# Optimization experiments

Hardware: AMD Instinct MI355X
Metric: run time of the kernel (lower is better)

The kernel has to match this reference:

```python
import jax, jax.numpy as jnp
import numpy as np

N = 100_000      # nodes
E = 1_600_000    # edges (avg degree 16)
IN = 128         # in_features
F = 64           # out_features
H = 1            # num_heads (module's broadcasting only valid for H==1)
S = 1            # num_samples
SLOPE = 0.2      # leaky relu negative slope


def setup_inputs() -> dict:
    key = jax.random.key(0)
    ks = jax.random.split(key, 6)
    feat = jax.random.normal(ks[0], (N, IN), jnp.float32)
    src = jax.random.randint(ks[1], (E,), 0, N)
    dst = jax.random.randint(ks[2], (E,), 0, N)
    noise = jax.random.normal(ks[3], (E, S, H, 1), jnp.float32)  # rsample noise
    W_fc = jax.random.normal(ks[4], (IN, H * F), jnp.float32) / np.sqrt(IN)
    W_post = jax.random.normal(ks[5], (F, 4), jnp.float32) / np.sqrt(F)
    b_post = jnp.zeros((4,), jnp.float32)
    bias = jnp.zeros((H, F), jnp.float32)
    return dict(feat=feat, W_fc=W_fc, W_post=W_post, b_post=b_post,
                bias=bias, noise=noise, src=src, dst=dst)


def reference(feat, W_fc, W_post, b_post, bias, noise, src, dst):
    # node projection: [N, IN] -> [N, H, F]
    h = (feat @ W_fc).reshape(N, H, F)
    # posterior params: [N, H, 4] -> four [N, H, 1]
    pp = h @ W_post + b_post
    loc_l, loc_r, lsl, lsr = jnp.split(pp, 4, axis=-1)
    # per-edge u_add_v gathers
    loc_e = loc_l[src] + loc_r[dst]                       # [E, H, 1]
    loc_e = jnp.where(loc_e >= 0, loc_e, SLOPE * loc_e)   # leaky relu
    scale_e = jnp.exp(lsl[src] + lsr[dst])                # [E, H, 1]
    # reparameterized sample: [E, S, H, 1]
    e = loc_e[:, None] + scale_e[:, None] * noise
    # edge softmax over incoming edges of each dst node
    emax = jax.ops.segment_max(e, dst, num_segments=N)
    e_exp = jnp.exp(e - emax[dst])
    esum = jax.ops.segment_sum(e_exp, dst, num_segments=N)
    a = e_exp / esum[dst]                                 # [E, S, H, 1]
    a = jnp.swapaxes(a, 1, -1)                            # [E, 1, H, S]
    # u_mul_e then scatter-sum to dst: [E, H, F, 1] * [E, 1, H, S]
    m = h[src][..., None] * a                             # [E, H, F, S] (H==1)
    rst = jax.ops.segment_sum(m, dst, num_segments=N)     # [N, H, F, S]
    return rst + bias[..., None]
```

## Files before the change

### kernel.cpp

```cpp
#include <hip/hip_runtime.h>
#include <math.h>

#define NSLOPE 0.2f
#define ASTRIDE 136
#define CSH 10
#define NCB 128
#define EPB 2048
#define K4T 512
#define EPT 4
#define FSPLIT 16
#define SCH 1152

typedef __attribute__((ext_vector_type(8))) short bf16x8;
typedef __attribute__((ext_vector_type(4))) short bf16x4;
typedef __attribute__((ext_vector_type(4))) float f32x4;

__device__ __forceinline__ unsigned short f2bf(float x) {
    unsigned u = __float_as_uint(x);
    u += 0x7fffu + ((u >> 16) & 1u);
    return (unsigned short)(u >> 16);
}

__global__ __launch_bounds__(128) void kW(const float* __restrict__ wfc,
                                          const float* __restrict__ wpost,
                                          float4* __restrict__ wc) {
    __shared__ float wp_s[256];
    int t = threadIdx.x;
    wp_s[t] = wpost[t];
    wp_s[128 + t] = wpost[128 + t];
    __syncthreads();
    float a0 = 0.f, a1 = 0.f, a2 = 0.f, a3 = 0.f;
    for (int n = 0; n < 64; n++) {
        float w = wfc[t * 64 + n];
        a0 += w * wp_s[n * 4 + 0]; a1 += w * wp_s[n * 4 + 1];
        a2 += w * wp_s[n * 4 + 2]; a3 += w * wp_s[n * 4 + 3];
    }
    float4 o; o.x = a0; o.y = a1; o.z = a2; o.w = a3;
    wc[t] = o;
}

__global__ __launch_bounds__(256) void k1_mfma(
    const float* __restrict__ feat, const float* __restrict__ wfc,
    float4* __restrict__ h_g, int n)
{
    __shared__ unsigned short a_s[64 * ASTRIDE];
    __shared__ unsigned short b_s[64 * ASTRIDE];
    int t = threadIdx.x;
    int row0 = blockIdx.x * 64;
    for (int i = t; i < 2048; i += 256) {
        int row = i >> 5, c4 = (i & 31) * 4;
        float4 f = {0.f, 0.f, 0.f, 0.f};
        if (row0 + row < n) f = ((const float4*)(feat + (long)(row0 + row) * 128))[i & 31];
        bf16x4 b4;
        b4.x = (short)f2bf(f.x); b4.y = (short)f2bf(f.y);
        b4.z = (short)f2bf(f.z); b4.w = (short)f2bf(f.w);
        *(bf16x4*)(a_s + row * ASTRIDE + c4) = b4;
    }
    for (int i = t; i < 2048; i += 256) {
        int k = i >> 4, n0 = (i & 15) * 4;
        float4 f = ((const float4*)wfc)[i];
        b_s[(n0 + 0) * ASTRIDE + k] = f2bf(f.x);
        b_s[(n0 + 1) * ASTRIDE + k] = f2bf(f.y);
        b_s[(n0 + 2) * ASTRIDE + k] = f2bf(f.z);
        b_s[(n0 + 3) * ASTRIDE + k] = f2bf(f.w);
    }
    __syncthreads();
    int lane = t & 63, wv = t >> 6;
    int c = lane & 15, quad = lane >> 4;
    f32x4 acc[4] = {{0.f,0.f,0.f,0.f},{0.f,0.f,0.f,0.f},{0.f,0.f,0.f,0.f},{0.f,0.f,0.f,0.f}};
    int arow = wv * 16 + c;
    #pragma unroll
    for (int kb = 0; kb < 4; kb++) {
        int ko = kb * 32 + quad * 8;
        bf16x8 af = *(const bf16x8*)(a_s + arow * ASTRIDE + ko);
        #pragma unroll
        for (int tt = 0; tt < 4; tt++) {
            bf16x8 bf = *(const bf16x8*)(b_s + (tt * 16 + c) * ASTRIDE + ko);
            acc[tt] = __builtin_amdgcn_mfma_f32_16x16x32_bf16(af, bf, acc[tt], 0, 0, 0);
        }
    }
    __syncthreads();
    unsigned short* h_s = a_s;
    #pragma unroll
    for (int tt = 0; tt < 4; tt++)
        #pragma unroll
        for (int r = 0; r < 4; r++)
            h_s[(wv * 16 + quad * 4 + r) * 64 + tt * 16 + c] = f2bf(acc[tt][r]);
    __syncthreads();
    for (int i = t; i < 512; i += 256) {
        int row = i >> 3;
        if (row0 + row < n)
            h_g[(long)(row0 + row) * 8 + (i & 7)] = *(const float4*)(h_s + row * 64 + (i & 7) * 8);
    }
}

__global__ __launch_bounds__(256) void k1b_pp(
    const float* __restrict__ feat, const float4* __restrict__ wc,
    const float* __restrict__ bpost, float4* __restrict__ pp,
    int* __restrict__ gcnt, int* __restrict__ fcnt, int NC, int N)
{
    int gid = blockIdx.x * 256 + threadIdx.x;
    if (gid < NC) gcnt[gid] = 0;
    if (gid < NC * 16) fcnt[gid] = 0;
    int wid = gid >> 6;
    int lane = threadIdx.x & 63;
    if (wid >= N) return;
    const float* fr = feat + (long)wid * 128;
    float f0 = fr[lane], f1 = fr[64 + lane];
    float4 w0 = wc[lane], w1 = wc[64 + lane];
    float p0 = f0 * w0.x + f1 * w1.x;
    float p1 = f0 * w0.y + f1 * w1.y;
    float p2 = f0 * w0.z + f1 * w1.z;
    float p3 = f0 * w0.w + f1 * w1.w;
    #pragma unroll
    for (int off = 1; off < 64; off <<= 1) {
        p0 += __shfl_xor(p0, off);
        p1 += __shfl_xor(p1, off);
        p2 += __shfl_xor(p2, off);
        p3 += __shfl_xor(p3, off);
    }
    if (lane == 0) {
        float4 bp = *((const float4*)bpost);
        float4 o;
        o.x = p0 + bp.x; o.y = p1 + bp.y; o.z = p2 + bp.z; o.w = p3 + bp.w;
        pp[wid] = o;
    }
}

__global__ __launch_bounds__(K4T) void k4a(
    const int* __restrict__ src, const int* __restrict__ dst,
    const float* __restrict__ noise, const float4* __restrict__ pp,
    int* __restrict__ gcnt, float2* __restrict__ cbuf, int E, int NC, int CCAP)
{
    __shared__ float    s_ev[EPB];
    __shared__ unsigned s_key[EPB];
    __shared__ unsigned char s_bin[EPB];
    __shared__ int hist[NCB], lbase[NCB], lcur[NCB], gdelta[NCB];
    __shared__ int wtot;
    int t = threadIdx.x;
    long e0 = (long)blockIdx.x * EPB;
    int d[EPT]; bool ok[EPT];
    for (int i = t; i < NCB; i += K4T) hist[i] = 0;
    __syncthreads();
    #pragma unroll
    for (int u = 0; u < EPT; u++) {
        long e = e0 + t + u * K4T;
        ok[u] = e < E;
        d[u] = ok[u] ? __builtin_nontemporal_load(dst + e) : 0;
        if (ok[u]) atomicAdd(&hist[d[u] >> CSH], 1);
    }
    __syncthreads();
    int v = (t < NCB) ? hist[t] : 0;
    int inc = v;
    #pragma unroll
    for (int off = 1; off < 64; off <<= 1) {
        int u2 = __shfl_up(inc, off);
        if ((t & 63) >= off) inc += u2;
    }
    if (t == 63) wtot = inc;
    __syncthreads();
    if (t < NCB) {
        int base = (t >= 64) ? wtot : 0;
        int lb = inc - v + base;
        lbase[t] = lb; lcur[t] = lb;
        if (t < NC && v > 0) {
            int gb = atomicAdd(&gcnt[t], v);
            gdelta[t] = gb - lb;
        }
    }
    __syncthreads();
    #pragma unroll
    for (int u = 0; u < EPT; u++) {
        if (!ok[u]) continue;
        long e = e0 + t + u * K4T;
        int s = __builtin_nontemporal_load(src + e);
        float nz = __builtin_nontemporal_load(noise + e);
        float4 ps = pp[s], pd = pp[d[u]];
        float loc = ps.x + pd.y;
        loc = loc >= 0.f ? loc : NSLOPE * loc;
        float ev = loc + __expf(ps.z + pd.w) * nz;
        int bin = d[u] >> CSH;
        int pos = atomicAdd(&lcur[bin], 1);
        s_ev[pos] = ev;
        s_key[pos] = (unsigned)s | ((unsigned)(d[u] & 1023) << 17);
        s_bin[pos] = (unsigned char)bin;
    }
    __syncthreads();
    long rem = (long)E - e0;
    int btot = rem < EPB ? (int)rem : EPB;
    for (int i = t; i < btot; i += K4T) {
        int bin = s_bin[i];
        int gpos = gdelta[bin] + i;
        if (gpos < CCAP) {
            float2 r; r.x = s_ev[i]; r.y = __uint_as_float(s_key[i]);
            cbuf[(long)bin * CCAP + gpos] = r;
        }
    }
}

__global__ __launch_bounds__(256) void k4b(
    const int* __restrict__ gcnt, const float2* __restrict__ cbuf,
    int* __restrict__ fcnt, float2* __restrict__ fbuf, int CCAP, int FCAP)
{
    __shared__ float    s_ev[SCH], s_ev2[SCH];
    __shared__ unsigned s_key[SCH], s_sr2[SCH];
    __shared__ unsigned char s_sub[SCH], s_sub2[SCH];
    __shared__ int h16[16], b16[16], cur16[16], gd16[16];
    int t = threadIdx.x;
    int c = blockIdx.x >> 4, j = blockIdx.x & 15;
    int cnt = gcnt[c]; if (cnt > CCAP) cnt = CCAP;
    int chunk = (cnt + FSPLIT - 1) / FSPLIT;
    int i0 = j * chunk;
    int i1 = i0 + chunk; if (i1 > cnt) i1 = cnt;
    int n = i1 - i0; if (n < 0) n = 0;
    if (t < 16) { h16[t] = 0; cur16[t] = 0; }
    __syncthreads();
    for (int i = t; i < n; i += 256) {
        float2 r = cbuf[(long)c * CCAP + i0 + i];
        unsigned key = __float_as_uint(r.y);
        int sub = (key >> 23) & 15;
        s_ev[i] = r.x; s_key[i] = key; s_sub[i] = (unsigned char)sub;
        atomicAdd(&h16[sub], 1);
    }
    __syncthreads();
    if (t == 0) {
        int run = 0;
        #pragma unroll
        for (int p = 0; p < 16; p++) { b16[p] = run; run += h16[p]; }
    }
    __syncthreads();
    if (t < 16 && h16[t] > 0)
        gd16[t] = atomicAdd(&fcnt[c * 16 + t], h16[t]) - b16[t];
    __syncthreads();
    for (int i = t; i < n; i += 256) {
        int sub = s_sub[i];
        int pos = b16[sub] + atomicAdd(&cur16[sub], 1);
        unsigned key = s_key[i];
        unsigned s  = key & 0x1FFFFu;
        unsigned dl = (key >> 17) & 63u;
        s_ev2[pos] = s_ev[i];
        s_sr2[pos] = s | (dl << 26);
        s_sub2[pos] = (unsigned char)sub;
    }
    __syncthreads();
    for (int i = t; i < n; i += 256) {
        int sub = s_sub2[i];
        int gpos = gd16[sub] + i;
        if (gpos < FCAP) {
            float2 r; r.x = s_ev2[i]; r.y = __uint_as_float(s_sr2[i]);
            fbuf[(long)(c * 16 + sub) * FCAP + gpos] = r;
        }
    }
}

__global__ __launch_bounds__(256) void k56_node(
    const int* __restrict__ fcnt, const float2* __restrict__ fbuf,
    const uint4* __restrict__ h8, const float* __restrict__ bias,
    float4* __restrict__ out4, int FCAP, int N)
{
    __shared__ float    o_ev[1344 + 8];
    __shared__ unsigned o_sr[1344 + 8];
    __shared__ int c[64], ox[64], c2[64];
    int t = threadIdx.x;
    int b = blockIdx.x;
    int n0 = b << 6;
    int cnt = fcnt[b]; if (cnt > FCAP) cnt = FCAP;
    const float2* rp = fbuf + (long)b * FCAP;
    if (t < 64) { c[t] = 0; c2[t] = 0; }
    __syncthreads();
    for (int i = t; i < cnt; i += 256)
        atomicAdd(&c[__float_as_uint(rp[i].y) >> 26], 1);
    __syncthreads();
    if (t < 64) {
        int val = c[t], inc = val;
        #pragma unroll
        for (int off = 1; off < 64; off <<= 1) {
            int u = __shfl_up(inc, off);
            if (t >= off) inc += u;
        }
        ox[t] = inc - val;
    }
    __syncthreads();
    for (int i = t; i < cnt; i += 256) {
        float2 v = rp[i];
        unsigned pk = __float_as_uint(v.y);
        int dl = pk >> 26;
        int pos = ox[dl] + atomicAdd(&c2[dl], 1);
        o_ev[pos] = v.x;
        o_sr[pos] = pk & 0x03FFFFFFu;
    }
    __syncthreads();
    {
        int nn4 = t >> 2, q = t & 3;
        int cn = c[nn4];
        int i0 = ox[nn4];
        float m = -INFINITY;
        for (int i = q; i < cn; i += 4) m = fmaxf(m, o_ev[i0 + i]);
        m = fmaxf(m, __shfl_xor(m, 1));
        m = fmaxf(m, __shfl_xor(m, 2));
        float ss = 0.f;
        for (int i = q; i < cn; i += 4) {
            float w = __expf(o_ev[i0 + i] - m);
            o_ev[i0 + i] = w;
            ss += w;
        }
        ss += __shfl_xor(ss, 1);
        ss += __shfl_xor(ss, 2);
        float inv = 1.f / ss;
        for (int i = q; i < cn; i += 4) o_ev[i0 + i] *= inv;
    }
    __syncthreads();
    int lane = t & 63, wv = t >> 6;
    int ch = lane & 7, sub = lane >> 3;
    for (int r = 0; r < 16; r += 2) {
        int nnA = wv * 16 + r, nnB = nnA + 1;
        int nodeA = n0 + nnA, nodeB = n0 + nnB;
        int cA = (nodeA < N) ? c[nnA] : 0;
        int cB = (nodeB < N) ? c[nnB] : 0;
        int iA = ox[nnA], iB = ox[nnB];
        float a0[8] = {0.f,0.f,0.f,0.f,0.f,0.f,0.f,0.f};
        float a1[8] = {0.f,0.f,0.f,0.f,0.f,0.f,0.f,0.f};
        int mx = cA > cB ? cA : cB;
        for (int jb = 0; jb < mx; jb += 16) {
            bool vA0 = (jb + sub) < cA, vA1 = (jb + 8 + sub) < cA;
            bool vB0 = (jb + sub) < cB, vB1 = (jb + 8 + sub) < cB;
            int jA0 = vA0 ? iA + jb + sub     : 0;
            int jA1 = vA1 ? iA + jb + 8 + sub : 0;
            int jB0 = vB0 ? iB + jb + sub     : 0;
            int jB1 = vB1 ? iB + jb + 8 + sub : 0;
            float wA0 = vA0 ? o_ev[jA0] : 0.f; int sA0 = vA0 ? (int)o_sr[jA0] : 0;
            float wA1 = vA1 ? o_ev[jA1] : 0.f; int sA1 = vA1 ? (int)o_sr[jA1] : 0;
            float wB0 = vB0 ? o_ev[jB0] : 0.f; int sB0 = vB0 ? (int)o_sr[jB0] : 0;
            float wB1 = vB1 ? o_ev[jB1] : 0.f; int sB1 = vB1 ? (int)o_sr[jB1] : 0;
            uint4 pA0 = h8[(long)sA0 * 8 + ch];
            uint4 pA1 = h8[(long)sA1 * 8 + ch];
            uint4 pB0 = h8[(long)sB0 * 8 + ch];
            uint4 pB1 = h8[(long)sB1 * 8 + ch];
            a0[0] += wA0 * __uint_as_float(pA0.x << 16);
            a0[1] += wA0 * __uint_as_float(pA0.x & 0xffff0000u);
            a0[2] += wA0 * __uint_as_float(pA0.y << 16);
            a0[3] += wA0 * __uint_as_float(pA0.y & 0xffff0000u);
            a0[4] += wA0 * __uint_as_float(pA0.z << 16);
            a0[5] += wA0 * __uint_as_float(pA0.z & 0xffff0000u);
            a0[6] += wA0 * __uint_as_float(pA0.w << 16);
            a0[7] += wA0 * __uint_as_float(pA0.w & 0xffff0000u);
            a0[0] += wA1 * __uint_as_float(pA1.x << 16);
            a0[1] += wA1 * __uint_as_float(pA1.x & 0xffff0000u);
            a0[2] += wA1 * __uint_as_float(pA1.y << 16);
            a0[3] += wA1 * __uint_as_float(pA1.y & 0xffff0000u);
            a0[4] += wA1 * __uint_as_float(pA1.z << 16);
            a0[5] += wA1 * __uint_as_float(pA1.z & 0xffff0000u);
            a0[6] += wA1 * __uint_as_float(pA1.w << 16);
            a0[7] += wA1 * __uint_as_float(pA1.w & 0xffff0000u);
            a1[0] += wB0 * __uint_as_float(pB0.x << 16);
            a1[1] += wB0 * __uint_as_float(pB0.x & 0xffff0000u);
            a1[2] += wB0 * __uint_as_float(pB0.y << 16);
            a1[3] += wB0 * __uint_as_float(pB0.y & 0xffff0000u);
            a1[4] += wB0 * __uint_as_float(pB0.z << 16);
            a1[5] += wB0 * __uint_as_float(pB0.z & 0xffff0000u);
            a1[6] += wB0 * __uint_as_float(pB0.w << 16);
            a1[7] += wB0 * __uint_as_float(pB0.w & 0xffff0000u);
            a1[0] += wB1 * __uint_as_float(pB1.x << 16);
            a1[1] += wB1 * __uint_as_float(pB1.x & 0xffff0000u);
            a1[2] += wB1 * __uint_as_float(pB1.y << 16);
            a1[3] += wB1 * __uint_as_float(pB1.y & 0xffff0000u);
            a1[4] += wB1 * __uint_as_float(pB1.z << 16);
            a1[5] += wB1 * __uint_as_float(pB1.z & 0xffff0000u);
            a1[6] += wB1 * __uint_as_float(pB1.w << 16);
            a1[7] += wB1 * __uint_as_float(pB1.w & 0xffff0000u);
        }
        #pragma unroll
        for (int off = 8; off < 64; off <<= 1)
            #pragma unroll
            for (int i = 0; i < 8; i++) {
                a0[i] += __shfl_xor(a0[i], off);
                a1[i] += __shfl_xor(a1[i], off);
            }
        if (sub == 0) {
            const float* bl = bias + ch * 8;
            if (nodeA < N) {
                f32x4 o0, o1;
                o0[0] = a0[0] + bl[0]; o0[1] = a0[1] + bl[1]; o0[2] = a0[2] + bl[2]; o0[3] = a0[3] + bl[3];
                o1[0] = a0[4] + bl[4]; o1[1] = a0[5] + bl[5]; o1[2] = a0[6] + bl[6]; o1[3] = a0[7] + bl[7];
                __builtin_nontemporal_store(o0, (f32x4*)(out4 + (long)nodeA * 16 + ch * 2));
                __builtin_nontemporal_store(o1, (f32x4*)(out4 + (long)nodeA * 16 + ch * 2 + 1));
            }
            if (nodeB < N) {
                f32x4 o0, o1;
                o0[0] = a1[0] + bl[0]; o0[1] = a1[1] + bl[1]; o0[2] = a1[2] + bl[2]; o0[3] = a1[3] + bl[3];
                o1[0] = a1[4] + bl[4]; o1[1] = a1[5] + bl[5]; o1[2] = a1[6] + bl[6]; o1[3] = a1[7] + bl[7];
                __builtin_nontemporal_store(o0, (f32x4*)(out4 + (long)nodeB * 16 + ch * 2));
                __builtin_nontemporal_store(o1, (f32x4*)(out4 + (long)nodeB * 16 + ch * 2 + 1));
            }
        }
    }
}

extern "C" void kernel_launch(void* const* d_in, const int* in_sizes, int n_in,
                              void* d_out, int out_size, void* d_ws, size_t ws_size,
                              hipStream_t stream) {
    const float* feat  = (const float*)d_in[0];
    const float* wfc   = (const float*)d_in[1];
    const float* wpost = (const float*)d_in[2];
    const float* bpost = (const float*)d_in[3];
    const float* bias  = (const float*)d_in[4];
    const float* noise = (const float*)d_in[5];
    const int*   src   = (const int*)d_in[6];
    const int*   dst   = (const int*)d_in[7];
    int N = in_sizes[0] / 128;
    int E = in_sizes[6];
    int NC = (N + 1023) >> 10;
    int NB = (N + 63) >> 6;
    int ECB = (E + NC - 1) / NC;
    int CCAP = (ECB + 8 * (int)sqrtf((float)ECB) + 71) & ~7;
    int EB  = (int)((long)E * 64 / N);
    int FCAP = (EB + 8 * (int)sqrtf((float)EB) + 39) & ~7;
    if (FCAP > 1344) FCAP = 1344;

    float*  ws   = (float*)d_ws;
    float2* cbuf = (float2*)ws;
    float2* fbuf = (float2*)(ws + (size_t)2 * NC * CCAP);
    float*  h    = ws + (size_t)2 * NC * CCAP + (size_t)2 * NB * FCAP;
    float4* pp   = (float4*)(h + (size_t)32 * N);
    int*    gcnt = (int*)(h + (size_t)32 * N + (size_t)4 * N);
    int*    fcnt = gcnt + 256;
    float4* wc   = (float4*)(fcnt + 2048);

    hipLaunchKernelGGL(kW, dim3(1), dim3(128), 0, stream, wfc, wpost, wc);
    hipLaunchKernelGGL(k1_mfma, dim3((N + 63) / 64), dim3(256), 0, stream,
                       feat, wfc, (float4*)h, N);
    hipLaunchKernelGGL(k1b_pp, dim3((N + 3) / 4), dim3(256), 0, stream,
                       feat, wc, bpost, pp, gcnt, fcnt, NC, N);
    hipLaunchKernelGGL(k4a, dim3((E + EPB - 1) / EPB), dim3(K4T), 0, stream,
                       src, dst, noise, pp, gcnt, cbuf, E, NC, CCAP);
    hipLaunchKernelGGL(k4b, dim3(NC * FSPLIT), dim3(256), 0, stream,
                       gcnt, cbuf, fcnt, fbuf, CCAP, FCAP);
    hipLaunchKernelGGL(k56_node, dim3(NB), dim3(256), 0, stream,
                       fcnt, fbuf, (const uint4*)h, bias, (float4*)d_out, FCAP, N);
}
```

Before: 256.1 us.

## Overlap bucket atomics, cache records in registers, process four nodes per gather pass

Halves the edge-bucketing block size, so blocks are smaller and more numerous. It also defers the global gcnt atomic so its latency overlaps the per-edge compute before the next barrier. In the node kernel, fbuf records are loaded once into registers and reused for both the histogram and scatter passes instead of being read twice from global memory. The aggregation loop now handles four destination nodes per iteration, giving eight independent h8 gathers in flight, which raises register pressure. The register cache assumes at most 1536 records per bucket (6 per thread).

```diff
diff --git a/kernel.cpp b/kernel.cpp
--- a/kernel.cpp
+++ b/kernel.cpp
@@ -5,8 +5,8 @@
 #define ASTRIDE 136
 #define CSH 10
 #define NCB 128
-#define EPB 2048
-#define K4T 512
+#define EPB 1024
+#define K4T 256
 #define EPT 4
 #define FSPLIT 16
 #define SCH 1152
@@ -135,7 +135,7 @@
     __shared__ float    s_ev[EPB];
     __shared__ unsigned s_key[EPB];
     __shared__ unsigned char s_bin[EPB];
-    __shared__ int hist[NCB], lbase[NCB], lcur[NCB], gdelta[NCB];
+    __shared__ int hist[NCB], lcur[NCB], gdelta[NCB];
     __shared__ int wtot;
     int t = threadIdx.x;
     long e0 = (long)blockIdx.x * EPB;
@@ -159,16 +159,15 @@
     }
     if (t == 63) wtot = inc;
     __syncthreads();
+    int lb = 0;
     if (t < NCB) {
         int base = (t >= 64) ? wtot : 0;
-        int lb = inc - v + base;
-        lbase[t] = lb; lcur[t] = lb;
-        if (t < NC && v > 0) {
-            int gb = atomicAdd(&gcnt[t], v);
-            gdelta[t] = gb - lb;
-        }
-    }
-    __syncthreads();
+        lb = inc - v + base;
+        lcur[t] = lb;
+    }
+    __syncthreads();
+    int gb = 0;
+    if (t < NC && v > 0) gb = atomicAdd(&gcnt[t], v);
     #pragma unroll
     for (int u = 0; u < EPT; u++) {
         if (!ok[u]) continue;
@@ -185,6 +184,7 @@
         s_key[pos] = (unsigned)s | ((unsigned)(d[u] & 1023) << 17);
         s_bin[pos] = (unsigned char)bin;
     }
+    if (t < NC && v > 0) gdelta[t] = gb - lb;
     __syncthreads();
     long rem = (long)E - e0;
     int btot = rem < EPB ? (int)rem : EPB;
@@ -268,8 +268,15 @@
     const float2* rp = fbuf + (long)b * FCAP;
     if (t < 64) { c[t] = 0; c2[t] = 0; }
     __syncthreads();
-    for (int i = t; i < cnt; i += 256)
-        atomicAdd(&c[__float_as_uint(rp[i].y) >> 26], 1);
+    float2 rec[6];
+    #pragma unroll
+    for (int j = 0; j < 6; j++) {
+        int i = t + j * 256;
+        if (i < cnt) {
+            rec[j] = rp[i];
+            atomicAdd(&c[__float_as_uint(rec[j].y) >> 26], 1);
+        }
+    }
     __syncthreads();
     if (t < 64) {
         int val = c[t], inc = val;
@@ -281,13 +288,16 @@
         ox[t] = inc - val;
     }
     __syncthreads();
-    for (int i = t; i < cnt; i += 256) {
-        float2 v = rp[i];
-        unsigned pk = __float_as_uint(v.y);
-        int dl = pk >> 26;
-        int pos = ox[dl] + atomicAdd(&c2[dl], 1);
-        o_ev[pos] = v.x;
-        o_sr[pos] = pk & 0x03FFFFFFu;
+    #pragma unroll
+    for (int j = 0; j < 6; j++) {
+        int i = t + j * 256;
+        if (i < cnt) {
+            unsigned pk = __float_as_uint(rec[j].y);
+            int dl = pk >> 26;
+            int pos = ox[dl] + atomicAdd(&c2[dl], 1);
+            o_ev[pos] = rec[j].x;
+            o_sr[pos] = pk & 0x03FFFFFFu;
+        }
     }
     __syncthreads();
     {
@@ -312,85 +322,70 @@
     __syncthreads();
     int lane = t & 63, wv = t >> 6;
     int ch = lane & 7, sub = lane >> 3;
-    for (int r = 0; r < 16; r += 2) {
-        int nnA = wv * 16 + r, nnB = nnA + 1;
-        int nodeA = n0 + nnA, nodeB = n0 + nnB;
-        int cA = (nodeA < N) ? c[nnA] : 0;
-        int cB = (nodeB < N) ? c[nnB] : 0;
-        int iA = ox[nnA], iB = ox[nnB];
-        float a0[8] = {0.f,0.f,0.f,0.f,0.f,0.f,0.f,0.f};
-        float a1[8] = {0.f,0.f,0.f,0.f,0.f,0.f,0.f,0.f};
-        int mx = cA > cB ? cA : cB;
+    for (int r = 0; r < 16; r += 4) {
+        int cX[4], iX[4];
+        #pragma unroll
+        for (int q = 0; q < 4; q++) {
+            int nn = wv * 16 + r + q;
+            cX[q] = (n0 + nn < N) ? c[nn] : 0;
+            iX[q] = ox[nn];
+        }
+        float acc[4][8];
+        #pragma unroll
+        for (int q = 0; q < 4; q++)
+            #pragma unroll
+            for (int i = 0; i < 8; i++) acc[q][i] = 0.f;
+        int mx01 = cX[0] > cX[1] ? cX[0] : cX[1];
+        int mx23 = cX[2] > cX[3] ? cX[2] : cX[3];
+        int mx = mx01 > mx23 ? mx01 : mx23;
         for (int jb = 0; jb < mx; jb += 16) {
-            bool vA0 = (jb + sub) < cA, vA1 = (jb + 8 + sub) < cA;
-            bool vB0 = (jb + sub) < cB, vB1 = (jb + 8 + sub) < cB;
-            int jA0 = vA0 ? iA + jb + sub     : 0;
-            int jA1 = vA1 ? iA + jb + 8 + sub : 0;
-            int jB0 = vB0 ? iB + jb + sub     : 0;
-            int jB1 = vB1 ? iB + jb + 8 + sub : 0;
-            float wA0 = vA0 ? o_ev[jA0] : 0.f; int sA0 = vA0 ? (int)o_sr[jA0] : 0;
-            float wA1 = vA1 ? o_ev[jA1] : 0.f; int sA1 = vA1 ? (int)o_sr[jA1] : 0;
-            float wB0 = vB0 ? o_ev[jB0] : 0.f; int sB0 = vB0 ? (int)o_sr[jB0] : 0;
-            float wB1 = vB1 ? o_ev[jB1] : 0.f; int sB1 = vB1 ? (int)o_sr[jB1] : 0;
-            uint4 pA0 = h8[(long)sA0 * 8 + ch];
-            uint4 pA1 = h8[(long)sA1 * 8 + ch];
-            uint4 pB0 = h8[(long)sB0 * 8 + ch];
-            uint4 pB1 = h8[(long)sB1 * 8 + ch];
-            a0[0] += wA0 * __uint_as_float(pA0.x << 16);
-            a0[1] += wA0 * __uint_as_float(pA0.x & 0xffff0000u);
-            a0[2] += wA0 * __uint_as_float(pA0.y << 16);
-            a0[3] += wA0 * __uint_as_float(pA0.y & 0xffff0000u);
-            a0[4] += wA0 * __uint_as_float(pA0.z << 16);
-            a0[5] += wA0 * __uint_as_float(pA0.z & 0xffff0000u);
-            a0[6] += wA0 * __uint_as_float(pA0.w << 16);
-            a0[7] += wA0 * __uint_as_float(pA0.w & 0xffff0000u);
-            a0[0] += wA1 * __uint_as_float(pA1.x << 16);
-            a0[1] += wA1 * __uint_as_float(pA1.x & 0xffff0000u);
-            a0[2] += wA1 * __uint_as_float(pA1.y << 16);
-            a0[3] += wA1 * __uint_as_float(pA1.y & 0xffff0000u);
-            a0[4] += wA1 * __uint_as_float(pA1.z << 16);
-            a0[5] += wA1 * __uint_as_float(pA1.z & 0xffff0000u);
-            a0[6] += wA1 * __uint_as_float(pA1.w << 16);
-            a0[7] += wA1 * __uint_as_float(pA1.w & 0xffff0000u);
-            a1[0] += wB0 * __uint_as_float(pB0.x << 16);
-            a1[1] += wB0 * __uint_as_float(pB0.x & 0xffff0000u);
-            a1[2] += wB0 * __uint_as_float(pB0.y << 16);
-            a1[3] += wB0 * __uint_as_float(pB0.y & 0xffff0000u);
-            a1[4] += wB0 * __uint_as_float(pB0.z << 16);
-            a1[5] += wB0 * __uint_as_float(pB0.z & 0xffff0000u);
-            a1[6] += wB0 * __uint_as_float(pB0.w << 16);
-            a1[7] += wB0 * __uint_as_float(pB0.w & 0xffff0000u);
-            a1[0] += wB1 * __uint_as_float(pB1.x << 16);
-            a1[1] += wB1 * __uint_as_float(pB1.x & 0xffff0000u);
-            a1[2] += wB1 * __uint_as_float(pB1.y << 16);
-            a1[3] += wB1 * __uint_as_float(pB1.y & 0xffff0000u);
-            a1[4] += wB1 * __uint_as_float(pB1.z << 16);
-            a1[5] += wB1 * __uint_as_float(pB1.z & 0xffff0000u);
-            a1[6] += wB1 * __uint_as_float(pB1.w << 16);
-            a1[7] += wB1 * __uint_as_float(pB1.w & 0xffff0000u);
+            #pragma unroll
+            for (int q = 0; q < 4; q++) {
+                bool v0 = (jb + sub) < cX[q], v1 = (jb + 8 + sub) < cX[q];
+                int j0 = v0 ? iX[q] + jb + sub     : 0;
+                int j1 = v1 ? iX[q] + jb + 8 + sub : 0;
+                float w0 = v0 ? o_ev[j0] : 0.f; int s0 = v0 ? (int)o_sr[j0] : 0;
+                float w1 = v1 ? o_ev[j1] : 0.f; int s1 = v1 ? (int)o_sr[j1] : 0;
+                uint4 p0 = h8[(long)s0 * 8 + ch];
+                uint4 p1 = h8[(long)s1 * 8 + ch];
+                acc[q][0] += w0 * __uint_as_float(p0.x << 16);
+                acc[q][1] += w0 * __uint_as_float(p0.x & 0xffff0000u);
+                acc[q][2] += w0 * __uint_as_float(p0.y << 16);
+                acc[q][3] += w0 * __uint_as_float(p0.y & 0xffff0000u);
+                acc[q][4] += w0 * __uint_as_float(p0.z << 16);
+                acc[q][5] += w0 * __uint_as_float(p0.z & 0xffff0000u);
+                acc[q][6] += w0 * __uint_as_float(p0.w << 16);
+                acc[q][7] += w0 * __uint_as_float(p0.w & 0xffff0000u);
+                acc[q][0] += w1 * __uint_as_float(p1.x << 16);
+                acc[q][1] += w1 * __uint_as_float(p1.x & 0xffff0000u);
+                acc[q][2] += w1 * __uint_as_float(p1.y << 16);
+                acc[q][3] += w1 * __uint_as_float(p1.y & 0xffff0000u);
+                acc[q][4] += w1 * __uint_as_float(p1.z << 16);
+                acc[q][5] += w1 * __uint_as_float(p1.z & 0xffff0000u);
+                acc[q][6] += w1 * __uint_as_float(p1.w << 16);
+                acc[q][7] += w1 * __uint_as_float(p1.w & 0xffff0000u);
+            }
         }
         #pragma unroll
         for (int off = 8; off < 64; off <<= 1)
             #pragma unroll
-            for (int i = 0; i < 8; i++) {
-                a0[i] += __shfl_xor(a0[i], off);
-                a1[i] += __shfl_xor(a1[i], off);
-            }
+            for (int q = 0; q < 4; q++)
+                #pragma unroll
+                for (int i = 0; i < 8; i++) acc[q][i] += __shfl_xor(acc[q][i], off);
         if (sub == 0) {
             const float* bl = bias + ch * 8;
-            if (nodeA < N) {
-                f32x4 o0, o1;
-                o0[0] = a0[0] + bl[0]; o0[1] = a0[1] + bl[1]; o0[2] = a0[2] + bl[2]; o0[3] = a0[3] + bl[3];
-                o1[0] = a0[4] + bl[4]; o1[1] = a0[5] + bl[5]; o1[2] = a0[6] + bl[6]; o1[3] = a0[7] + bl[7];
-                __builtin_nontemporal_store(o0, (f32x4*)(out4 + (long)nodeA * 16 + ch * 2));
-                __builtin_nontemporal_store(o1, (f32x4*)(out4 + (long)nodeA * 16 + ch * 2 + 1));
-            }
-            if (nodeB < N) {
-                f32x4 o0, o1;
-                o0[0] = a1[0] + bl[0]; o0[1] = a1[1] + bl[1]; o0[2] = a1[2] + bl[2]; o0[3] = a1[3] + bl[3];
-                o1[0] = a1[4] + bl[4]; o1[1] = a1[5] + bl[5]; o1[2] = a1[6] + bl[6]; o1[3] = a1[7] + bl[7];
-                __builtin_nontemporal_store(o0, (f32x4*)(out4 + (long)nodeB * 16 + ch * 2));
-                __builtin_nontemporal_store(o1, (f32x4*)(out4 + (long)nodeB * 16 + ch * 2 + 1));
+            #pragma unroll
+            for (int q = 0; q < 4; q++) {
+                int node = n0 + wv * 16 + r + q;
+                if (node < N) {
+                    f32x4 o0, o1;
+                    o0[0] = acc[q][0] + bl[0]; o0[1] = acc[q][1] + bl[1];
+                    o0[2] = acc[q][2] + bl[2]; o0[3] = acc[q][3] + bl[3];
+                    o1[0] = acc[q][4] + bl[4]; o1[1] = acc[q][5] + bl[5];
+                    o1[2] = acc[q][6] + bl[6]; o1[3] = acc[q][7] + bl[7];
+                    __builtin_nontemporal_store(o0, (f32x4*)(out4 + (long)node * 16 + ch * 2));
+                    __builtin_nontemporal_store(o1, (f32x4*)(out4 + (long)node * 16 + ch * 2 + 1));
+                }
             }
         }
     }
```

Measured after the change: 273.4 us. 6.8% more time.
